# Performance work log

Measured on AMD Instinct MI355X. Metric: run time of the kernel, lower is better.

Reference implementation:

```python
import jax, jax.numpy as jnp
import numpy as np

SIZE = 512
FEATURES = 16
IN_FEATURES = 16
BATCH = 8192
EXCLUSIVE = 1  # module init arg exclusive=True


def setup_inputs() -> dict:
    key = jax.random.key(0)
    k1, k2, k3, k4 = jax.random.split(key, 4)
    inputs = jax.random.normal(k1, (BATCH, IN_FEATURES), dtype=jnp.float32)
    cache = jax.random.normal(k2, (BATCH, SIZE, IN_FEATURES), dtype=jnp.float32)
    kernel = jax.random.normal(k3, (SIZE * IN_FEATURES, SIZE * FEATURES), dtype=jnp.float32)
    bias = jax.random.normal(k4, (SIZE, FEATURES), dtype=jnp.float32)
    index = 300
    return {"inputs": inputs, "cache": cache, "kernel": kernel, "bias": bias, "index": index}


def reference(inputs, cache, kernel, bias, index):
    # Faithful translation of FastMaskedDense1D.update_site.
    batch, in_features = inputs.shape
    size, features = bias.shape
    size_i = index + 1

    # scatter the new input site into the cache (index - exclusive >= 0 branch)
    if index - EXCLUSIVE >= 0:
        cache = cache.at[:, index - EXCLUSIVE, :].set(inputs)

    # cached inputs up to the current site, flattened: (batch, size_i*in_features)
    cache_i = cache[:, :size_i, :].reshape(batch, size_i * in_features)

    # dynamic slice of the kernel for output site `index`: (size_i, in_features, features)
    kernel_i = kernel.reshape(size, in_features, size, features)[:size_i, :, index, :]

    # triu(ones, exclusive) kron ones mask, sliced at [:size_i, :, index, :]:
    # row j is 1 iff index >= j + exclusive
    mask = (jnp.arange(size_i) <= index - EXCLUSIVE).astype(kernel_i.dtype)
    kernel_i = (kernel_i * mask[:, None, None]).reshape(size_i * in_features, features)

    y_i = cache_i @ kernel_i + bias[index, :]  # (batch, features)
    return y_i
```

## Files before the change

### kernel.cpp

```cpp
#include <hip/hip_runtime.h>


#define EXCLUSIVE 1
#define SIZEV     512
#define NF        16
#define NIF       16
#define KROW      (SIZEV * NF)
#define CROW      (SIZEV * NIF)
#define MB        16
#define KC        256
#define SA        272

__device__ __forceinline__ void fma4(float4& a, float s, float4 b) {
    a.x = fmaf(s, b.x, a.x);
    a.y = fmaf(s, b.y, a.y);
    a.z = fmaf(s, b.z, a.z);
    a.w = fmaf(s, b.w, a.w);
}

__device__ __forceinline__ float4 red4(float4 v, int m) {
    v.x += __shfl_xor(v.x, m, 64);
    v.y += __shfl_xor(v.y, m, 64);
    v.z += __shfl_xor(v.z, m, 64);
    v.w += __shfl_xor(v.w, m, 64);
    return v;
}

__global__ __launch_bounds__(256) void pack_k(
    const float* __restrict__ kern,
    const int*   __restrict__ idxp,
    float*       __restrict__ kp)
{
    const int index = *idxp;
    const int jc = index - EXCLUSIVE + 1;
    const int KT = (jc > 0) ? jc * NIF : 0;
    const int t  = blockIdx.x * blockDim.x + threadIdx.x;
    const int r  = t >> 2;
    const int q  = t & 3;
    if (r < KT) {
        const float4 v = *(const float4*)(kern + (size_t)r * KROW + (size_t)index * NF + 4 * q);
        *(float4*)(kp + (size_t)r * NF + 4 * q) = v;
    }
}

__global__ __launch_bounds__(256) void fmd_kernel(
    const float* __restrict__ inputs,
    const float* __restrict__ cache,
    const float* __restrict__ kp,
    const float* __restrict__ bias,
    const int*   __restrict__ idxp,
    float*       __restrict__ out)
{
    __shared__ float A[2][MB * SA];

    const int index = *idxp;
    const int jc = index - EXCLUSIVE + 1;
    const int KM = (jc > 0) ? (jc - 1) * NIF : 0;
    const int NC = (KM + KC - 1) / KC;

    const int tid  = threadIdx.x;
    const int lane = tid & 63;
    const int w    = tid >> 6;
    const int kq   = lane & 15;
    const int rq   = lane >> 4;
    const int rh   = w >> 1;
    const int fh   = w & 1;
    const int row0 = blockIdx.x * MB;

    const int lr0 = rh * 8 + rq;
    const int lr1 = lr0 + 4;

    float4 acc00 = {0,0,0,0}, acc01 = {0,0,0,0};
    float4 acc10 = {0,0,0,0}, acc11 = {0,0,0,0};

    const float4* cvec  = (const float4*)cache;
    const float*  kbase = kp + (size_t)fh * 8;

    float4 st[4];

    if (NC > 0) {
        #pragma unroll
        for (int p = 0; p < 4; ++p)
            st[p] = cvec[(size_t)(row0 + w + 4*p) * (CROW/4) + lane];
        #pragma unroll
        for (int p = 0; p < 4; ++p)
            *(float4*)&A[0][(w + 4*p) * SA + lane * 4] = st[p];

        for (int c = 0; c < NC; ++c) {
            const int k0 = c * KC;
            if (c + 1 < NC) {
                const int k4 = (k0 + KC) >> 2;
                #pragma unroll
                for (int p = 0; p < 4; ++p)
                    st[p] = cvec[(size_t)(row0 + w + 4*p) * (CROW/4) + k4 + lane];
            }
            __syncthreads();

            const int buf  = c & 1;
            const int kend = min(KC, KM - k0);
            const int nt   = kend >> 4;
            const float* Ab = &A[buf][0];

            #pragma unroll 4
            for (int t = 0; t < nt; ++t) {
                const int kk = kq + 16 * t;
                float a0 = Ab[lr0 * SA + kk];
                float a1 = Ab[lr1 * SA + kk];
                const float* kptr = kbase + (size_t)(k0 + kk) * NF;
                float4 kv0 = *(const float4*)kptr;
                float4 kv1 = *(const float4*)(kptr + 4);
                fma4(acc00, a0, kv0); fma4(acc01, a0, kv1);
                fma4(acc10, a1, kv0); fma4(acc11, a1, kv1);
            }

            if (c + 1 < NC) {
                const int b2 = (c + 1) & 1;
                #pragma unroll
                for (int p = 0; p < 4; ++p)
                    *(float4*)&A[b2][(w + 4*p) * SA + lane * 4] = st[p];
            }
        }
    }

    if (jc > 0) {
        const float* kptr = kbase + (size_t)((jc - 1) * NIF + kq) * NF;
        float4 kv0 = *(const float4*)kptr;
        float4 kv1 = *(const float4*)(kptr + 4);
        float in0 = inputs[(size_t)(row0 + lr0) * NIF + kq];
        float in1 = inputs[(size_t)(row0 + lr1) * NIF + kq];
        fma4(acc00, in0, kv0); fma4(acc01, in0, kv1);
        fma4(acc10, in1, kv0); fma4(acc11, in1, kv1);
    }

    #pragma unroll
    for (int m = 1; m <= 8; m <<= 1) {
        acc00 = red4(acc00, m); acc01 = red4(acc01, m);
        acc10 = red4(acc10, m); acc11 = red4(acc11, m);
    }

    if (kq < 4) {
        const int rp = kq >> 1;
        const int qp = kq & 1;
        float4 v = (rp == 0) ? (qp == 0 ? acc00 : acc01)
                             : (qp == 0 ? acc10 : acc11);
        const int row  = row0 + lr0 + 4 * rp;
        const int fcol = fh * 8 + qp * 4;
        float4 b4 = *(const float4*)&bias[(size_t)index * NF + fcol];
        v.x += b4.x; v.y += b4.y; v.z += b4.z; v.w += b4.w;
        *(float4*)&out[(size_t)row * NF + fcol] = v;
    }
}

extern "C" void kernel_launch(void* const* d_in, const int* in_sizes, int n_in,
                              void* d_out, int out_size, void* d_ws, size_t ws_size,
                              hipStream_t stream) {
    const float* inputs = (const float*)d_in[0];
    const float* cache  = (const float*)d_in[1];
    const float* kern   = (const float*)d_in[2];
    const float* bias   = (const float*)d_in[3];
    const int*   idxp   = (const int*)d_in[4];
    float*       out    = (float*)d_out;
    float*       kp     = (float*)d_ws;

    const int batch = in_sizes[0] / NIF;
    const int grid  = batch / MB;

    pack_k<<<(SIZEV * NIF * 4) / 256, 256, 0, stream>>>(kern, idxp, kp);
    fmd_kernel<<<grid, 256, 0, stream>>>(inputs, cache, kp, bias, idxp, out);
}
```

Baseline: 503.3 us.

## Stage packed kernel slice in LDS and split K across 512 threads

The packed kernel slice is now double-buffered in shared memory next to the cache tile, replacing per-thread global loads inside the inner loop. Blocks grow to 512 threads, with two wave groups splitting the K dimension and combining partial sums through a small shared-memory reduction. The K chunk shrinks to 128, and the pack kernel zero-pads up to a chunk multiple so the staged loads stay in bounds. This adds a barrier and extra LDS traffic, and workload per block is unchanged for a bandwidth-bound cache stream.

```diff
diff --git a/kernel.cpp b/kernel.cpp
--- a/kernel.cpp
+++ b/kernel.cpp
@@ -8,8 +8,9 @@
 #define KROW      (SIZEV * NF)
 #define CROW      (SIZEV * NIF)
 #define MB        16
-#define KC        256
-#define SA        272
+#define KC        128
+#define SA        136
+#define SK        20
 
 __device__ __forceinline__ void fma4(float4& a, float s, float4 b) {
     a.x = fmaf(s, b.x, a.x);
@@ -34,16 +35,19 @@
     const int index = *idxp;
     const int jc = index - EXCLUSIVE + 1;
     const int KT = (jc > 0) ? jc * NIF : 0;
+    const int KTpad = (KT + KC - 1) & ~(KC - 1);
     const int t  = blockIdx.x * blockDim.x + threadIdx.x;
     const int r  = t >> 2;
     const int q  = t & 3;
-    if (r < KT) {
-        const float4 v = *(const float4*)(kern + (size_t)r * KROW + (size_t)index * NF + 4 * q);
+    if (r < KTpad) {
+        float4 v = {0.f, 0.f, 0.f, 0.f};
+        if (r < KT)
+            v = *(const float4*)(kern + (size_t)r * KROW + (size_t)index * NF + 4 * q);
         *(float4*)(kp + (size_t)r * NF + 4 * q) = v;
     }
 }
 
-__global__ __launch_bounds__(256) void fmd_kernel(
+__global__ __launch_bounds__(512) void fmd_kernel(
     const float* __restrict__ inputs,
     const float* __restrict__ cache,
     const float* __restrict__ kp,
@@ -51,7 +55,9 @@
     const int*   __restrict__ idxp,
     float*       __restrict__ out)
 {
-    __shared__ float A[2][MB * SA];
+    __shared__ float A [2][MB * SA];
+    __shared__ float Kl[2][KC * SK];
+    __shared__ float Red[MB * NF];
 
     const int index = *idxp;
     const int jc = index - EXCLUSIVE + 1;
@@ -63,69 +69,71 @@
     const int w    = tid >> 6;
     const int kq   = lane & 15;
     const int rq   = lane >> 4;
-    const int rh   = w >> 1;
     const int fh   = w & 1;
+    const int rh   = (w >> 1) & 1;
+    const int ks   = w >> 2;
     const int row0 = blockIdx.x * MB;
 
     const int lr0 = rh * 8 + rq;
     const int lr1 = lr0 + 4;
 
+    const int arow = tid >> 5;
+    const int ac4  = tid & 31;
+    const int krow = tid >> 2;
+    const int kc4  = tid & 3;
+
     float4 acc00 = {0,0,0,0}, acc01 = {0,0,0,0};
     float4 acc10 = {0,0,0,0}, acc11 = {0,0,0,0};
 
-    const float4* cvec  = (const float4*)cache;
-    const float*  kbase = kp + (size_t)fh * 8;
+    const float4* cvec = (const float4*)cache;
+    const float4* kpv  = (const float4*)kp;
 
-    float4 st[4];
+    float4 stA, stK;
 
     if (NC > 0) {
-        #pragma unroll
-        for (int p = 0; p < 4; ++p)
-            st[p] = cvec[(size_t)(row0 + w + 4*p) * (CROW/4) + lane];
-        #pragma unroll
-        for (int p = 0; p < 4; ++p)
-            *(float4*)&A[0][(w + 4*p) * SA + lane * 4] = st[p];
+        stA = cvec[(size_t)(row0 + arow) * (CROW/4) + ac4];
+        stK = kpv[4 * krow + kc4];
+        *(float4*)&A [0][arow * SA + 4 * ac4] = stA;
+        *(float4*)&Kl[0][krow * SK + 4 * kc4] = stK;
 
         for (int c = 0; c < NC; ++c) {
             const int k0 = c * KC;
             if (c + 1 < NC) {
-                const int k4 = (k0 + KC) >> 2;
-                #pragma unroll
-                for (int p = 0; p < 4; ++p)
-                    st[p] = cvec[(size_t)(row0 + w + 4*p) * (CROW/4) + k4 + lane];
+                stA = cvec[(size_t)(row0 + arow) * (CROW/4) + ((k0 + KC) >> 2) + ac4];
+                stK = kpv[4 * (k0 + KC + krow) + kc4];
             }
             __syncthreads();
 
             const int buf  = c & 1;
             const int kend = min(KC, KM - k0);
-            const int nt   = kend >> 4;
-            const float* Ab = &A[buf][0];
+            const int nt   = (kend - 16 * ks + 31) >> 5;
+            const float* Ab = &A [buf][0];
+            const float* Kb = &Kl[buf][0];
 
             #pragma unroll 4
             for (int t = 0; t < nt; ++t) {
-                const int kk = kq + 16 * t;
+                const int kk = kq + 32 * t + 16 * ks;
                 float a0 = Ab[lr0 * SA + kk];
                 float a1 = Ab[lr1 * SA + kk];
-                const float* kptr = kbase + (size_t)(k0 + kk) * NF;
-                float4 kv0 = *(const float4*)kptr;
-                float4 kv1 = *(const float4*)(kptr + 4);
+                const float* kp4 = &Kb[kk * SK + fh * 8];
+                float4 kv0 = *(const float4*)kp4;
+                float4 kv1 = *(const float4*)(kp4 + 4);
                 fma4(acc00, a0, kv0); fma4(acc01, a0, kv1);
                 fma4(acc10, a1, kv0); fma4(acc11, a1, kv1);
             }
 
             if (c + 1 < NC) {
                 const int b2 = (c + 1) & 1;
-                #pragma unroll
-                for (int p = 0; p < 4; ++p)
-                    *(float4*)&A[b2][(w + 4*p) * SA + lane * 4] = st[p];
+                *(float4*)&A [b2][arow * SA + 4 * ac4] = stA;
+                *(float4*)&Kl[b2][krow * SK + 4 * kc4] = stK;
             }
         }
     }
 
-    if (jc > 0) {
-        const float* kptr = kbase + (size_t)((jc - 1) * NIF + kq) * NF;
-        float4 kv0 = *(const float4*)kptr;
-        float4 kv1 = *(const float4*)(kptr + 4);
+    if (jc > 0 && ks == 0) {
+        const float* kg = kp + (size_t)((jc - 1) * NIF + kq) * NF + fh * 8;
+        float4 kv0 = *(const float4*)kg;
+        float4 kv1 = *(const float4*)(kg + 4);
         float in0 = inputs[(size_t)(row0 + lr0) * NIF + kq];
         float in1 = inputs[(size_t)(row0 + lr1) * NIF + kq];
         fma4(acc00, in0, kv0); fma4(acc01, in0, kv1);
@@ -135,19 +143,25 @@
     #pragma unroll
     for (int m = 1; m <= 8; m <<= 1) {
         acc00 = red4(acc00, m); acc01 = red4(acc01, m);
-        acc10 = red4(acc10, m); acc11 = red4(acc11, m);
+        acc10 = red4(acc10, m); acc10 = acc10; acc11 = red4(acc11, m);
     }
 
-    if (kq < 4) {
-        const int rp = kq >> 1;
-        const int qp = kq & 1;
-        float4 v = (rp == 0) ? (qp == 0 ? acc00 : acc01)
-                             : (qp == 0 ? acc10 : acc11);
-        const int row  = row0 + lr0 + 4 * rp;
-        const int fcol = fh * 8 + qp * 4;
+    const int rp = kq >> 1;
+    const int qp = kq & 1;
+    float4 v = (rp == 0) ? (qp == 0 ? acc00 : acc01)
+                         : (qp == 0 ? acc10 : acc11);
+    const int brow = lr0 + 4 * rp;
+    const int fcol = fh * 8 + 4 * qp;
+
+    if (ks == 1 && kq < 4)
+        *(float4*)&Red[brow * NF + fcol] = v;
+    __syncthreads();
+    if (ks == 0 && kq < 4) {
+        float4 o  = *(const float4*)&Red[brow * NF + fcol];
         float4 b4 = *(const float4*)&bias[(size_t)index * NF + fcol];
-        v.x += b4.x; v.y += b4.y; v.z += b4.z; v.w += b4.w;
-        *(float4*)&out[(size_t)row * NF + fcol] = v;
+        v.x += o.x + b4.x; v.y += o.y + b4.y;
+        v.z += o.z + b4.z; v.w += o.w + b4.w;
+        *(float4*)&out[(size_t)(row0 + brow) * NF + fcol] = v;
     }
 }
 
@@ -166,5 +180,5 @@
     const int grid  = batch / MB;
 
     pack_k<<<(SIZEV * NIF * 4) / 256, 256, 0, stream>>>(kern, idxp, kp);
-    fmd_kernel<<<grid, 256, 0, stream>>>(inputs, cache, kp, bias, idxp, out);
+    fmd_kernel<<<grid, 512, 0, stream>>>(inputs, cache, kp, bias, idxp, out);
 }
```

Result: faster. 438.1 us (-13.0%).
